# Optimization experiments

Hardware: AMD Instinct MI355X
Metric: run time of the kernel (lower is better)

The kernel has to match this reference:

```python
import jax, jax.numpy as jnp
import numpy as np

N_NODES = 100000
N_EDGES = 1_600_000
D_IN = 128
D_OUT = 128


def setup_inputs() -> dict:
    key = jax.random.key(0)
    k1, k2, k3, k4 = jax.random.split(key, 4)
    x = jax.random.normal(k1, (N_NODES, D_IN), dtype=jnp.float32)
    adj = jax.random.randint(k2, (2, N_EDGES), 0, N_NODES, dtype=jnp.int64)
    # eqx.nn.Linear-style init: U(-1/sqrt(in), 1/sqrt(in))
    lim = 1.0 / np.sqrt(D_IN)
    W = jax.random.uniform(k3, (D_OUT, D_IN), minval=-lim, maxval=lim, dtype=jnp.float32)
    b = jax.random.uniform(k4, (D_OUT,), minval=-lim, maxval=lim, dtype=jnp.float32)
    return {"x": x, "adj": adj, "W": W, "b": b}


def reference(x, adj, W, b):
    n = x.shape[0]
    s, r = adj[0], adj[1]
    ones = jnp.ones(s.shape, dtype=x.dtype)
    sender_degree = jax.ops.segment_sum(ones, s, num_segments=n)    # [n]
    receiver_degree = jax.ops.segment_sum(ones, r, num_segments=n)  # [n]
    # linear (dropout is identity at p=0)
    h = x @ W.T + b                                                 # [n, D_OUT]
    # symmetric degree normalization: rescale senders, scatter-add to receivers, rescale receivers
    h = h * jax.lax.rsqrt(jnp.maximum(sender_degree, 1.0))[:, None]
    h = jax.ops.segment_sum(h[s], r, num_segments=n)                # gather + scatter-add
    h = h * jax.lax.rsqrt(jnp.maximum(receiver_degree, 1.0))[:, None]
    h = jax.nn.silu(h)
    return (h, adj)
```

## Files before the change

### kernel.cpp

```cpp
#include <hip/hip_runtime.h>
#include <hip/hip_bf16.h>
#include <hip/hip_fp16.h>

typedef __attribute__((ext_vector_type(8))) short short8;
typedef __attribute__((ext_vector_type(4))) float floatx4;

#define DFEAT 128
#define BCAP 5120
#define WSTR 136

__device__ __forceinline__ int clampi(int v, int lo, int hi) {
    return v < lo ? lo : (v > hi ? hi : v);
}
__device__ __forceinline__ ushort f2bf(float f) {
    unsigned u = __float_as_uint(f);
    unsigned r = (u + 0x7FFFu + ((u >> 16) & 1u)) >> 16;
    return (ushort)r;
}
__device__ __forceinline__ float bf2f(ushort u) {
    return __uint_as_float(((unsigned)u) << 16);
}
__device__ __forceinline__ float h16tof(ushort hb) {
    __half_raw hr; hr.x = hb;
    return __half2float((__half)hr);
}
__device__ __forceinline__ unsigned f2bf8_sw(float f) {
    __half h = __float2half(f);
    __half_raw hr = (__half_raw)h;
    unsigned u = (unsigned)hr.x;
    return (u + 0x7Fu + ((u >> 8) & 1u)) >> 8;
}
__device__ __forceinline__ unsigned packbf8x4(float4 v) {
#if __has_builtin(__builtin_amdgcn_cvt_pk_bf8_f32)
    int lo = __builtin_amdgcn_cvt_pk_bf8_f32(v.x, v.y, 0, false);
    int full = __builtin_amdgcn_cvt_pk_bf8_f32(v.z, v.w, lo, true);
    return (unsigned)full;
#else
    return f2bf8_sw(v.x) | (f2bf8_sw(v.y) << 8) | (f2bf8_sw(v.z) << 16) | (f2bf8_sw(v.w) << 24);
#endif
}
__device__ __forceinline__ float2 bf8x2tof(int w) {
#if __has_builtin(__builtin_amdgcn_cvt_pk_f32_bf8)
    typedef __attribute__((ext_vector_type(2))) float f2v;
    f2v r = __builtin_amdgcn_cvt_pk_f32_bf8(w, false);
    float2 o; o.x = r[0]; o.y = r[1];
    return o;
#else
    float2 o;
    o.x = h16tof((ushort)((w & 0xFF) << 8));
    o.y = h16tof((ushort)(w & 0xFF00));
    return o;
#endif
}

__device__ __forceinline__ int ldS(const int* adj, int f, int E, int e) {
    return f ? adj[2 * (size_t)e] : adj[e];
}
__device__ __forceinline__ int ldR(const int* adj, int f, int E, int e) {
    return f ? adj[2 * ((size_t)E + e)] : adj[(size_t)E + e];
}

__global__ __launch_bounds__(512) void k_front(const float* __restrict__ x,
                                               unsigned* __restrict__ xs, int n32, int staged,
                                               const float* __restrict__ W, unsigned* __restrict__ Wb,
                                               const int* __restrict__ adj, int* __restrict__ flag_g,
                                               int* __restrict__ scur, int* __restrict__ rcur,
                                               unsigned char* __restrict__ sbuf, unsigned* __restrict__ rbuf,
                                               int E, int N, int NBK, int SG) {
    int t = threadIdx.x;
    int b = blockIdx.x;
    if (b < SG) {
        if (b == 0) {
            for (int i = t; i < 8192; i += 512) {
                float2 v = ((const float2*)W)[i];
                Wb[i] = (unsigned)f2bf(v.x) | ((unsigned)f2bf(v.y) << 16);
            }
        }
        if (staged) {
            int stride = SG * 512;
            for (int i = b * 512 + t; i < n32; i += stride)
                xs[i] = packbf8x4(((const float4*)x)[i]);
        }
        return;
    }
    __shared__ int hs[512], hr[512], bs[512], br[512];
    __shared__ int fsh;
    int pb = b - SG;
    int PB = gridDim.x - SG;
    if (t < 64) {
        int nz = 0;
        for (int i = t; i < 256; i += 64) nz |= adj[2 * i + 1];
        #pragma unroll
        for (int off = 32; off > 0; off >>= 1) nz |= __shfl_down(nz, off);
        if (t == 0) { fsh = (nz == 0) ? 1 : 0; if (pb == 0) flag_g[0] = fsh; }
    }
    hs[t] = 0; hr[t] = 0;
    __syncthreads();
    int f = fsh;
    int chunk = (E + PB - 1) / PB;
    int e0 = pb * chunk;
    int e1 = min(E, e0 + chunk);
    for (int e = e0 + t; e < e1; e += 512) {
        int s = clampi(ldS(adj, f, E, e), 0, N - 1);
        int r = clampi(ldR(adj, f, E, e), 0, N - 1);
        atomicAdd(&hs[s >> 8], 1);
        atomicAdd(&hr[r >> 8], 1);
    }
    __syncthreads();
    for (int i = t; i < NBK; i += 512) {
        bs[i] = hs[i] ? atomicAdd(&scur[i], hs[i]) : 0;
        br[i] = hr[i] ? atomicAdd(&rcur[i], hr[i]) : 0;
    }
    __syncthreads();
    for (int e = e0 + t; e < e1; e += 512) {
        int s = clampi(ldS(adj, f, E, e), 0, N - 1);
        int r = clampi(ldR(adj, f, E, e), 0, N - 1);
        int ps = atomicAdd(&bs[s >> 8], 1);
        if (ps < BCAP) sbuf[(size_t)(s >> 8) * BCAP + ps] = (unsigned char)(s & 255);
        int pr = atomicAdd(&br[r >> 8], 1);
        if (pr < BCAP) rbuf[(size_t)(r >> 8) * BCAP + pr] = ((unsigned)(r & 255) << 17) | (unsigned)s;
    }
}

__global__ __launch_bounds__(256) void k_invs(const unsigned char* __restrict__ sbuf,
                                              const int* __restrict__ scur,
                                              float* __restrict__ inv_s, int N) {
    __shared__ int h[256];
    int b = blockIdx.x, t = threadIdx.x;
    int sc = min(scur[b], BCAP);
    const unsigned char* sb = sbuf + (size_t)b * BCAP;
    h[t] = 0;
    __syncthreads();
    for (int i = t; i < sc; i += 256) atomicAdd(&h[sb[i]], 1);
    __syncthreads();
    int node = (b << 8) + t;
    if (node < N) inv_s[node] = rsqrtf(fmaxf((float)h[t], 1.0f));
}

__global__ __launch_bounds__(256) void k_sort(unsigned* __restrict__ rbuf,
                                              const int* __restrict__ rcur,
                                              const float* __restrict__ inv_s,
                                              int* __restrict__ deg_r, int* __restrict__ startv,
                                              int N) {
    __shared__ unsigned pk[BCAP];
    __shared__ int h[256], off[256];
    int b = blockIdx.x, t = threadIdx.x;
    int node = (b << 8) + t;
    int cnt = min(rcur[b], BCAP);
    unsigned* rb = rbuf + (size_t)b * BCAP;
    for (int i = t; i < cnt; i += 256) pk[i] = rb[i];
    h[t] = 0;
    __syncthreads();
    for (int i = t; i < cnt; i += 256) atomicAdd(&h[pk[i] >> 17], 1);
    __syncthreads();
    int hv = h[t];
    off[t] = hv;
    __syncthreads();
    for (int o = 1; o < 256; o <<= 1) {
        int v = (t >= o) ? off[t - o] : 0;
        __syncthreads();
        off[t] += v;
        __syncthreads();
    }
    int excl = off[t] - hv;
    if (node < N) { deg_r[node] = hv; startv[node] = b * BCAP + excl; }
    __syncthreads();
    h[t] = excl;
    __syncthreads();
    for (int i = t; i < cnt; i += 256) {
        unsigned v = pk[i];
        int s = (int)(v & 0x1FFFFu);
        unsigned iv8 = f2bf8_sw(inv_s[clampi(s, 0, N - 1)]);
        int pos = atomicAdd(&h[v >> 17], 1);
        if (pos >= 0 && pos < cnt) rb[pos] = (v & 0x1FFFFu) | (iv8 << 24);
    }
}

__global__ __launch_bounds__(512) void k_back(const ushort* __restrict__ xs,
                                              const float* __restrict__ bias,
                                              const unsigned* __restrict__ Wb,
                                              const int* __restrict__ startv,
                                              const int* __restrict__ deg_r,
                                              const unsigned* __restrict__ esrc,
                                              float* __restrict__ out0, int N, int RB, int ntiles,
                                              const int* __restrict__ adj, const int* __restrict__ flag,
                                              float* __restrict__ out1, int n1) {
    __shared__ ushort Wt[128 * WSTR];
    __shared__ ushort At[32 * WSTR];
    __shared__ float csrow[32], invrow[32];
    int tid = threadIdx.x;

    if ((int)blockIdx.x >= ntiles) {
        int f = flag[0];
        int nb = gridDim.x - ntiles;
        for (int i = ((int)blockIdx.x - ntiles) * 512 + tid; i < n1; i += nb * 512) {
            int v = f ? adj[2 * (size_t)i] : adj[i];
            out1[i] = bf2f(f2bf((float)v));
        }
        return;
    }

    int m0 = blockIdx.x * 32;
    for (int i = tid; i < 8192; i += 512) {
        unsigned v = Wb[i];
        int row = i >> 6, col = (2 * i) & 127;
        *(unsigned*)(&Wt[row * WSTR + col]) = v;
    }

    int w = tid >> 6, d = tid & 63;
    #pragma unroll 1
    for (int k = 0; k < 4; ++k) {
        int nl = w * 4 + k;
        int node = m0 + nl;
        int cnt = 0, base = 0;
        if (node < N) {
            cnt = clampi(deg_r[node], 0, BCAP);
            base = clampi(startv[node], 0, RB - cnt);
        }
        cnt = __builtin_amdgcn_readfirstlane(cnt);
        base = __builtin_amdgcn_readfirstlane(base);
        const unsigned* ep = esrc + base;
        float a0 = 0.f, a1 = 0.f, cs = 0.f;
        int j = 0;
        for (; j + 7 < cnt; j += 8) {
            unsigned q0 = ep[j],     q1 = ep[j + 1], q2 = ep[j + 2], q3 = ep[j + 3];
            unsigned q4 = ep[j + 4], q5 = ep[j + 5], q6 = ep[j + 6], q7 = ep[j + 7];
            int r0 = (int)xs[((q0 & 0x1FFFFu) << 6) + d];
            int r1 = (int)xs[((q1 & 0x1FFFFu) << 6) + d];
            int r2 = (int)xs[((q2 & 0x1FFFFu) << 6) + d];
            int r3 = (int)xs[((q3 & 0x1FFFFu) << 6) + d];
            int r4 = (int)xs[((q4 & 0x1FFFFu) << 6) + d];
            int r5 = (int)xs[((q5 & 0x1FFFFu) << 6) + d];
            int r6 = (int)xs[((q6 & 0x1FFFFu) << 6) + d];
            int r7 = (int)xs[((q7 & 0x1FFFFu) << 6) + d];
            float v0 = h16tof((ushort)((q0 >> 16) & 0xFF00u));
            float v1 = h16tof((ushort)((q1 >> 16) & 0xFF00u));
            float v2 = h16tof((ushort)((q2 >> 16) & 0xFF00u));
            float v3 = h16tof((ushort)((q3 >> 16) & 0xFF00u));
            float v4 = h16tof((ushort)((q4 >> 16) & 0xFF00u));
            float v5 = h16tof((ushort)((q5 >> 16) & 0xFF00u));
            float v6 = h16tof((ushort)((q6 >> 16) & 0xFF00u));
            float v7 = h16tof((ushort)((q7 >> 16) & 0xFF00u));
            float2 f0 = bf8x2tof(r0), f1 = bf8x2tof(r1), f2 = bf8x2tof(r2), f3 = bf8x2tof(r3);
            float2 f4 = bf8x2tof(r4), f5 = bf8x2tof(r5), f6 = bf8x2tof(r6), f7 = bf8x2tof(r7);
            a0 += v0 * f0.x; a1 += v0 * f0.y;
            a0 += v1 * f1.x; a1 += v1 * f1.y;
            a0 += v2 * f2.x; a1 += v2 * f2.y;
            a0 += v3 * f3.x; a1 += v3 * f3.y;
            a0 += v4 * f4.x; a1 += v4 * f4.y;
            a0 += v5 * f5.x; a1 += v5 * f5.y;
            a0 += v6 * f6.x; a1 += v6 * f6.y;
            a0 += v7 * f7.x; a1 += v7 * f7.y;
            cs += ((v0 + v1) + (v2 + v3)) + ((v4 + v5) + (v6 + v7));
        }
        for (; j < cnt; ++j) {
            unsigned q0 = ep[j];
            float v0 = h16tof((ushort)((q0 >> 16) & 0xFF00u));
            float2 f0 = bf8x2tof((int)xs[((q0 & 0x1FFFFu) << 6) + d]);
            a0 += v0 * f0.x; a1 += v0 * f0.y;
            cs += v0;
        }
        ushort2 p; p.x = f2bf(a0); p.y = f2bf(a1);
        *(ushort2*)(&At[nl * WSTR + 2 * d]) = p;
        if (d == 0) {
            csrow[nl] = cs;
            invrow[nl] = rsqrtf(fmaxf((float)cnt, 1.0f));
        }
    }
    __syncthreads();

    int quad = d >> 4, r16 = d & 15;
    int rt = w & 1;
    short8 a[4];
    #pragma unroll
    for (int g = 0; g < 4; ++g)
        a[g] = *(const short8*)(&At[(rt * 16 + r16) * WSTR + g * 32 + quad * 8]);

    #pragma unroll
    for (int half = 0; half < 2; ++half) {
        int ct = (w >> 1) + half * 4;
        floatx4 acc = {0.f, 0.f, 0.f, 0.f};
        #pragma unroll
        for (int g = 0; g < 4; ++g) {
            short8 bb = *(const short8*)(&Wt[(ct * 16 + r16) * WSTR + g * 32 + quad * 8]);
            acc = __builtin_amdgcn_mfma_f32_16x16x32_bf16(a[g], bb, acc, 0, 0, 0);
        }
        int dcol = ct * 16 + r16;
        float bc = bias[dcol];
        #pragma unroll
        for (int g = 0; g < 4; ++g) {
            int ml = rt * 16 + quad * 4 + g;
            int grow = m0 + ml;
            if (grow < N) {
                float v = (acc[g] + csrow[ml] * bc) * invrow[ml];
                float z = v / (1.0f + __expf(-v));
                if (!(z > -50.0f && z < 50.0f)) z = 0.0f;
                out0[(size_t)grow * DFEAT + dcol] = z;
            }
        }
    }
}

__global__ __launch_bounds__(256) void k_aggregate_fb(const float* __restrict__ x,
                                                      const int* __restrict__ startv,
                                                      const int* __restrict__ deg_r,
                                                      const unsigned* __restrict__ esrc,
                                                      float* __restrict__ xa,
                                                      float* __restrict__ cvec, int N, int RB) {
    int node = blockIdx.x * 4 + (threadIdx.x >> 6);
    int d = threadIdx.x & 63;
    if (node >= N) return;
    int cnt = clampi(deg_r[node], 0, BCAP);
    int base = clampi(startv[node], 0, RB - cnt);
    cnt = __builtin_amdgcn_readfirstlane(cnt);
    base = __builtin_amdgcn_readfirstlane(base);
    const unsigned* ep = esrc + base;
    float a0 = 0.f, a1 = 0.f, cs = 0.f;
    for (int j = 0; j < cnt; ++j) {
        unsigned w0 = ep[j];
        int s0 = (int)(w0 & 0x1FFFFu);
        float v0 = h16tof((ushort)((w0 >> 16) & 0xFF00u));
        float2 f0 = ((const float2*)x)[(size_t)s0 * 64 + d];
        a0 += v0 * f0.x; a1 += v0 * f0.y;
        cs += v0;
    }
    float2 o; o.x = a0; o.y = a1;
    ((float2*)xa)[(size_t)node * 64 + d] = o;
    if (d == 0) cvec[node] = cs;
}

__global__ __launch_bounds__(256) void k_matmul_fb(float* __restrict__ xa,
                                                   const unsigned* __restrict__ Wb,
                                                   const float* __restrict__ bias,
                                                   const float* __restrict__ c,
                                                   const int* __restrict__ deg_r, int M) {
    __shared__ ushort Wt[128 * WSTR];
    __shared__ ushort At[64 * WSTR];
    int tid = threadIdx.x;
    int m0 = blockIdx.x * 64;
    for (int i = tid; i < 8192; i += 256) {
        unsigned v = Wb[i];
        int row = i >> 6, col = (2 * i) & 127;
        *(unsigned*)(&Wt[row * WSTR + col]) = v;
    }
    for (int i = tid; i < 4096; i += 256) {
        int row = i >> 6, col = (2 * i) & 127;
        int grow = m0 + row;
        float2 v;
        if (grow < M) v = ((const float2*)xa)[(size_t)grow * 64 + (col >> 1)];
        else { v.x = 0.f; v.y = 0.f; }
        ushort2 p; p.x = f2bf(v.x); p.y = f2bf(v.y);
        *(ushort2*)(&At[row * WSTR + col]) = p;
    }
    __syncthreads();
    int wid = tid >> 6, lane = tid & 63;
    int quad = lane >> 4, r16 = lane & 15;
    short8 a[4];
    #pragma unroll
    for (int g = 0; g < 4; ++g)
        a[g] = *(const short8*)(&At[(wid * 16 + r16) * WSTR + g * 32 + quad * 8]);
    int rbl = wid * 16 + quad * 4;
    float cg[4], invr[4];
    #pragma unroll
    for (int g = 0; g < 4; ++g) {
        int row = min(m0 + rbl + g, M - 1);
        cg[g] = c[row];
        invr[g] = rsqrtf(fmaxf((float)deg_r[row], 1.0f));
    }
    #pragma unroll
    for (int nt = 0; nt < 8; ++nt) {
        floatx4 acc = {0.f, 0.f, 0.f, 0.f};
        #pragma unroll
        for (int g = 0; g < 4; ++g) {
            short8 bb = *(const short8*)(&Wt[(nt * 16 + r16) * WSTR + g * 32 + quad * 8]);
            acc = __builtin_amdgcn_mfma_f32_16x16x32_bf16(a[g], bb, acc, 0, 0, 0);
        }
        int dcol = nt * 16 + r16;
        float bc = bias[dcol];
        #pragma unroll
        for (int g = 0; g < 4; ++g) {
            int grow = m0 + rbl + g;
            if (grow < M) {
                float v = (acc[g] + cg[g] * bc) * invr[g];
                float z = v / (1.0f + __expf(-v));
                if (!(z > -50.0f && z < 50.0f)) z = 0.0f;
                xa[(size_t)grow * DFEAT + dcol] = z;
            }
        }
    }
}

__global__ void k_adjcopy(const int* __restrict__ adj, const int* __restrict__ flag,
                          float* __restrict__ out, int n) {
    int i = blockIdx.x * 256 + threadIdx.x;
    if (i >= n) return;
    int f = flag[0];
    int v = f ? adj[2 * (size_t)i] : adj[i];
    out[i] = bf2f(f2bf((float)v));
}

extern "C" void kernel_launch(void* const* d_in, const int* in_sizes, int n_in,
                              void* d_out, int out_size, void* d_ws, size_t ws_size,
                              hipStream_t stream) {
    const float* x    = (const float*)d_in[0];
    const int*   adj  = (const int*)d_in[1];
    const float* W    = (const float*)d_in[2];
    const float* bias = (const float*)d_in[3];

    const int N = in_sizes[0] / DFEAT;
    const int E = (out_size - N * DFEAT) / 2;
    const int NBK = (N + 255) >> 8;
    const int N4 = ((N + 255) / 256) * 256;
    const int RB = NBK * BCAP;

    float* out  = (float*)d_out;
    float* out0 = out;
    float* out1 = out + (size_t)N * DFEAT;

    size_t xsB  = (size_t)N * DFEAT;
    size_t sbB  = ((size_t)NBK * BCAP + 255) & ~(size_t)255;
    size_t rbB  = (size_t)RB * 4;
    size_t metaB = (size_t)N4 * 16 + 8192;
    size_t need = xsB + sbB + rbB + metaB + 32768;
    int staged = (ws_size >= need) ? 1 : 0;

    unsigned char* sbuf;
    unsigned* rbuf;
    char* csr;
    ushort* xs = (ushort*)d_ws;
    if (staged) {
        sbuf = (unsigned char*)d_ws + xsB;
        rbuf = (unsigned*)((char*)d_ws + xsB + sbB);
        csr  = (char*)d_ws + xsB + sbB + rbB;
    } else {
        sbuf = (unsigned char*)d_out;
        rbuf = (unsigned*)out1;
        csr  = (char*)out1 + rbB;
    }
    float* inv_s  = (float*)csr;
    int*   deg_r  = (int*)(csr + (size_t)N4 * 4);
    int*   startv = (int*)(csr + (size_t)N4 * 8);
    float* cvec   = (float*)(csr + (size_t)N4 * 12);
    int*   bkt    = (int*)(csr + (size_t)N4 * 16);
    unsigned* Wb  = (unsigned*)(csr + metaB);
    int *scur = bkt, *rcur = bkt + 512, *flag = bkt + 1024;

    hipMemsetAsync(bkt, 0, 1028 * 4, stream);

    int SG = staged ? 512 : 1;
    int PB = 256;
    k_front<<<SG + PB, 512, 0, stream>>>(x, (unsigned*)xs, N * 32, staged, W, Wb, adj, flag,
                                         scur, rcur, sbuf, rbuf, E, N, NBK, SG);
    k_invs<<<NBK, 256, 0, stream>>>(sbuf, scur, inv_s, N);
    k_sort<<<NBK, 256, 0, stream>>>(rbuf, rcur, inv_s, deg_r, startv, N);

    if (staged) {
        int ntiles = (N + 31) / 32;
        k_back<<<ntiles + 256, 512, 0, stream>>>(xs, bias, Wb, startv, deg_r, rbuf,
                                                 out0, N, RB, ntiles, adj, flag, out1, 2 * E);
    } else {
        k_aggregate_fb<<<(N + 3) / 4, 256, 0, stream>>>(x, startv, deg_r, rbuf, out0, cvec, N, RB);
        k_matmul_fb<<<(N + 63) / 64, 256, 0, stream>>>(out0, Wb, bias, cvec, deg_r, N);
        k_adjcopy<<<(2 * E + 255) / 256, 256, 0, stream>>>(adj, flag, out1, 2 * E);
    }
}
```

Measured before the change: 233.4 us.

## Count sender degrees with global atomics, drop k_invs, read W from global

Sender degrees are now counted with direct global atomics in k_front, replacing the bucketed sender buffer and the separate k_invs kernel. The per-receiver coefficient sum moves into k_sort, so the aggregation loop in k_back no longer accumulates it. k_back stops staging W in shared memory, reading MFMA B operands straight from global/L2, and gets a launch bound of 512 threads with a minimum of 8 blocks to raise occupancy. The trade-off is 1.6M contended global atomics and uncached-in-LDS weight reads in exchange for one fewer kernel, less shared memory and higher occupancy.

```diff
diff --git a/kernel.cpp b/kernel.cpp
--- a/kernel.cpp
+++ b/kernel.cpp
@@ -64,8 +64,8 @@
                                                unsigned* __restrict__ xs, int n32, int staged,
                                                const float* __restrict__ W, unsigned* __restrict__ Wb,
                                                const int* __restrict__ adj, int* __restrict__ flag_g,
-                                               int* __restrict__ scur, int* __restrict__ rcur,
-                                               unsigned char* __restrict__ sbuf, unsigned* __restrict__ rbuf,
+                                               int* __restrict__ rcur, int* __restrict__ deg_s,
+                                               unsigned* __restrict__ rbuf,
                                                int E, int N, int NBK, int SG) {
     int t = threadIdx.x;
     int b = blockIdx.x;
@@ -83,7 +83,7 @@
         }
         return;
     }
-    __shared__ int hs[512], hr[512], bs[512], br[512];
+    __shared__ int hr[512], br[512];
     __shared__ int fsh;
     int pb = b - SG;
     int PB = gridDim.x - SG;
@@ -94,62 +94,48 @@
         for (int off = 32; off > 0; off >>= 1) nz |= __shfl_down(nz, off);
         if (t == 0) { fsh = (nz == 0) ? 1 : 0; if (pb == 0) flag_g[0] = fsh; }
     }
-    hs[t] = 0; hr[t] = 0;
+    hr[t] = 0;
     __syncthreads();
     int f = fsh;
     int chunk = (E + PB - 1) / PB;
     int e0 = pb * chunk;
     int e1 = min(E, e0 + chunk);
     for (int e = e0 + t; e < e1; e += 512) {
-        int s = clampi(ldS(adj, f, E, e), 0, N - 1);
         int r = clampi(ldR(adj, f, E, e), 0, N - 1);
-        atomicAdd(&hs[s >> 8], 1);
         atomicAdd(&hr[r >> 8], 1);
     }
     __syncthreads();
-    for (int i = t; i < NBK; i += 512) {
-        bs[i] = hs[i] ? atomicAdd(&scur[i], hs[i]) : 0;
+    for (int i = t; i < NBK; i += 512)
         br[i] = hr[i] ? atomicAdd(&rcur[i], hr[i]) : 0;
-    }
     __syncthreads();
     for (int e = e0 + t; e < e1; e += 512) {
         int s = clampi(ldS(adj, f, E, e), 0, N - 1);
         int r = clampi(ldR(adj, f, E, e), 0, N - 1);
-        int ps = atomicAdd(&bs[s >> 8], 1);
-        if (ps < BCAP) sbuf[(size_t)(s >> 8) * BCAP + ps] = (unsigned char)(s & 255);
+        atomicAdd(&deg_s[s], 1);
         int pr = atomicAdd(&br[r >> 8], 1);
         if (pr < BCAP) rbuf[(size_t)(r >> 8) * BCAP + pr] = ((unsigned)(r & 255) << 17) | (unsigned)s;
     }
 }
 
-__global__ __launch_bounds__(256) void k_invs(const unsigned char* __restrict__ sbuf,
-                                              const int* __restrict__ scur,
-                                              float* __restrict__ inv_s, int N) {
-    __shared__ int h[256];
-    int b = blockIdx.x, t = threadIdx.x;
-    int sc = min(scur[b], BCAP);
-    const unsigned char* sb = sbuf + (size_t)b * BCAP;
-    h[t] = 0;
-    __syncthreads();
-    for (int i = t; i < sc; i += 256) atomicAdd(&h[sb[i]], 1);
-    __syncthreads();
-    int node = (b << 8) + t;
-    if (node < N) inv_s[node] = rsqrtf(fmaxf((float)h[t], 1.0f));
-}
-
 __global__ __launch_bounds__(256) void k_sort(unsigned* __restrict__ rbuf,
                                               const int* __restrict__ rcur,
-                                              const float* __restrict__ inv_s,
+                                              const int* __restrict__ deg_s,
+                                              float* __restrict__ cvec,
                                               int* __restrict__ deg_r, int* __restrict__ startv,
                                               int N) {
-    __shared__ unsigned pk[BCAP];
+    __shared__ __align__(16) unsigned pk[BCAP];
     __shared__ int h[256], off[256];
+    __shared__ float csf[256];
     int b = blockIdx.x, t = threadIdx.x;
     int node = (b << 8) + t;
     int cnt = min(rcur[b], BCAP);
     unsigned* rb = rbuf + (size_t)b * BCAP;
-    for (int i = t; i < cnt; i += 256) pk[i] = rb[i];
+    int cnt4 = cnt >> 2;
+    const uint4* rb4 = (const uint4*)rb;
+    for (int i = t; i < cnt4; i += 256) ((uint4*)pk)[i] = rb4[i];
+    for (int i = (cnt4 << 2) + t; i < cnt; i += 256) pk[i] = rb[i];
     h[t] = 0;
+    csf[t] = 0.f;
     __syncthreads();
     for (int i = t; i < cnt; i += 256) atomicAdd(&h[pk[i] >> 17], 1);
     __syncthreads();
@@ -170,22 +156,27 @@
     for (int i = t; i < cnt; i += 256) {
         unsigned v = pk[i];
         int s = (int)(v & 0x1FFFFu);
-        unsigned iv8 = f2bf8_sw(inv_s[clampi(s, 0, N - 1)]);
+        int dg = deg_s[clampi(s, 0, N - 1)];
+        unsigned iv8 = f2bf8_sw(rsqrtf(fmaxf((float)dg, 1.0f)));
+        float vq = h16tof((ushort)(iv8 << 8));
+        atomicAdd(&csf[v >> 17], vq);
         int pos = atomicAdd(&h[v >> 17], 1);
         if (pos >= 0 && pos < cnt) rb[pos] = (v & 0x1FFFFu) | (iv8 << 24);
     }
-}
-
-__global__ __launch_bounds__(512) void k_back(const ushort* __restrict__ xs,
-                                              const float* __restrict__ bias,
-                                              const unsigned* __restrict__ Wb,
-                                              const int* __restrict__ startv,
-                                              const int* __restrict__ deg_r,
-                                              const unsigned* __restrict__ esrc,
-                                              float* __restrict__ out0, int N, int RB, int ntiles,
-                                              const int* __restrict__ adj, const int* __restrict__ flag,
-                                              float* __restrict__ out1, int n1) {
-    __shared__ ushort Wt[128 * WSTR];
+    __syncthreads();
+    if (node < N) cvec[node] = csf[t];
+}
+
+__global__ __launch_bounds__(512, 8) void k_back(const ushort* __restrict__ xs,
+                                                 const float* __restrict__ bias,
+                                                 const unsigned* __restrict__ Wb,
+                                                 const int* __restrict__ startv,
+                                                 const int* __restrict__ deg_r,
+                                                 const unsigned* __restrict__ esrc,
+                                                 const float* __restrict__ cvec,
+                                                 float* __restrict__ out0, int N, int RB, int ntiles,
+                                                 const int* __restrict__ adj, const int* __restrict__ flag,
+                                                 float* __restrict__ out1, int n1) {
     __shared__ ushort At[32 * WSTR];
     __shared__ float csrow[32], invrow[32];
     int tid = threadIdx.x;
@@ -201,12 +192,6 @@
     }
 
     int m0 = blockIdx.x * 32;
-    for (int i = tid; i < 8192; i += 512) {
-        unsigned v = Wb[i];
-        int row = i >> 6, col = (2 * i) & 127;
-        *(unsigned*)(&Wt[row * WSTR + col]) = v;
-    }
-
     int w = tid >> 6, d = tid & 63;
     #pragma unroll 1
     for (int k = 0; k < 4; ++k) {
@@ -220,7 +205,7 @@
         cnt = __builtin_amdgcn_readfirstlane(cnt);
         base = __builtin_amdgcn_readfirstlane(base);
         const unsigned* ep = esrc + base;
-        float a0 = 0.f, a1 = 0.f, cs = 0.f;
+        float a0 = 0.f, a1 = 0.f;
         int j = 0;
         for (; j + 7 < cnt; j += 8) {
             unsigned q0 = ep[j],     q1 = ep[j + 1], q2 = ep[j + 2], q3 = ep[j + 3];
@@ -251,19 +236,17 @@
             a0 += v5 * f5.x; a1 += v5 * f5.y;
             a0 += v6 * f6.x; a1 += v6 * f6.y;
             a0 += v7 * f7.x; a1 += v7 * f7.y;
-            cs += ((v0 + v1) + (v2 + v3)) + ((v4 + v5) + (v6 + v7));
         }
         for (; j < cnt; ++j) {
             unsigned q0 = ep[j];
             float v0 = h16tof((ushort)((q0 >> 16) & 0xFF00u));
             float2 f0 = bf8x2tof((int)xs[((q0 & 0x1FFFFu) << 6) + d]);
             a0 += v0 * f0.x; a1 += v0 * f0.y;
-            cs += v0;
         }
         ushort2 p; p.x = f2bf(a0); p.y = f2bf(a1);
         *(ushort2*)(&At[nl * WSTR + 2 * d]) = p;
         if (d == 0) {
-            csrow[nl] = cs;
+            csrow[nl] = (node < N) ? cvec[node] : 0.f;
             invrow[nl] = rsqrtf(fmaxf((float)cnt, 1.0f));
         }
     }
@@ -276,13 +259,14 @@
     for (int g = 0; g < 4; ++g)
         a[g] = *(const short8*)(&At[(rt * 16 + r16) * WSTR + g * 32 + quad * 8]);
 
+    const ushort* Wr = (const ushort*)Wb;
     #pragma unroll
     for (int half = 0; half < 2; ++half) {
         int ct = (w >> 1) + half * 4;
         floatx4 acc = {0.f, 0.f, 0.f, 0.f};
         #pragma unroll
         for (int g = 0; g < 4; ++g) {
-            short8 bb = *(const short8*)(&Wt[(ct * 16 + r16) * WSTR + g * 32 + quad * 8]);
+            short8 bb = *(const short8*)(Wr + ((ct * 16 + r16) << 7) + g * 32 + quad * 8);
             acc = __builtin_amdgcn_mfma_f32_16x16x32_bf16(a[g], bb, acc, 0, 0, 0);
         }
         int dcol = ct * 16 + r16;
@@ -305,8 +289,7 @@
                                                       const int* __restrict__ startv,
                                                       const int* __restrict__ deg_r,
                                                       const unsigned* __restrict__ esrc,
-                                                      float* __restrict__ xa,
-                                                      float* __restrict__ cvec, int N, int RB) {
+                                                      float* __restrict__ xa, int N, int RB) {
     int node = blockIdx.x * 4 + (threadIdx.x >> 6);
     int d = threadIdx.x & 63;
     if (node >= N) return;
@@ -315,18 +298,16 @@
     cnt = __builtin_amdgcn_readfirstlane(cnt);
     base = __builtin_amdgcn_readfirstlane(base);
     const unsigned* ep = esrc + base;
-    float a0 = 0.f, a1 = 0.f, cs = 0.f;
+    float a0 = 0.f, a1 = 0.f;
     for (int j = 0; j < cnt; ++j) {
         unsigned w0 = ep[j];
         int s0 = (int)(w0 & 0x1FFFFu);
         float v0 = h16tof((ushort)((w0 >> 16) & 0xFF00u));
         float2 f0 = ((const float2*)x)[(size_t)s0 * 64 + d];
         a0 += v0 * f0.x; a1 += v0 * f0.y;
-        cs += v0;
     }
     float2 o; o.x = a0; o.y = a1;
     ((float2*)xa)[(size_t)node * 64 + d] = o;
-    if (d == 0) cvec[node] = cs;
 }
 
 __global__ __launch_bounds__(256) void k_matmul_fb(float* __restrict__ xa,
@@ -418,48 +399,44 @@
     float* out1 = out + (size_t)N * DFEAT;
 
     size_t xsB  = (size_t)N * DFEAT;
-    size_t sbB  = ((size_t)NBK * BCAP + 255) & ~(size_t)255;
     size_t rbB  = (size_t)RB * 4;
-    size_t metaB = (size_t)N4 * 16 + 8192;
-    size_t need = xsB + sbB + rbB + metaB + 32768;
+    size_t metaB = (size_t)N4 * 16 + 4096 + 32768;
+    size_t need = xsB + rbB + metaB + 4096;
     int staged = (ws_size >= need) ? 1 : 0;
 
-    unsigned char* sbuf;
     unsigned* rbuf;
     char* csr;
     ushort* xs = (ushort*)d_ws;
     if (staged) {
-        sbuf = (unsigned char*)d_ws + xsB;
-        rbuf = (unsigned*)((char*)d_ws + xsB + sbB);
-        csr  = (char*)d_ws + xsB + sbB + rbB;
+        rbuf = (unsigned*)((char*)d_ws + xsB);
+        csr  = (char*)d_ws + xsB + rbB;
     } else {
-        sbuf = (unsigned char*)d_out;
         rbuf = (unsigned*)out1;
         csr  = (char*)out1 + rbB;
     }
-    float* inv_s  = (float*)csr;
-    int*   deg_r  = (int*)(csr + (size_t)N4 * 4);
-    int*   startv = (int*)(csr + (size_t)N4 * 8);
-    float* cvec   = (float*)(csr + (size_t)N4 * 12);
-    int*   bkt    = (int*)(csr + (size_t)N4 * 16);
-    unsigned* Wb  = (unsigned*)(csr + metaB);
-    int *scur = bkt, *rcur = bkt + 512, *flag = bkt + 1024;
-
-    hipMemsetAsync(bkt, 0, 1028 * 4, stream);
+    int*   ibase  = (int*)csr;
+    int*   deg_s  = ibase;
+    int*   rcur   = ibase + N4;
+    int*   flag   = ibase + N4 + 512;
+    int*   deg_r  = ibase + N4 + 1024;
+    int*   startv = deg_r + N4;
+    float* cvec   = (float*)(startv + N4);
+    unsigned* Wb  = (unsigned*)(cvec + N4);
+
+    hipMemsetAsync(deg_s, 0, (size_t)N4 * 4 + 4096, stream);
 
     int SG = staged ? 512 : 1;
     int PB = 256;
     k_front<<<SG + PB, 512, 0, stream>>>(x, (unsigned*)xs, N * 32, staged, W, Wb, adj, flag,
-                                         scur, rcur, sbuf, rbuf, E, N, NBK, SG);
-    k_invs<<<NBK, 256, 0, stream>>>(sbuf, scur, inv_s, N);
-    k_sort<<<NBK, 256, 0, stream>>>(rbuf, rcur, inv_s, deg_r, startv, N);
+                                         rcur, deg_s, rbuf, E, N, NBK, SG);
+    k_sort<<<NBK, 256, 0, stream>>>(rbuf, rcur, deg_s, cvec, deg_r, startv, N);
 
     if (staged) {
         int ntiles = (N + 31) / 32;
-        k_back<<<ntiles + 256, 512, 0, stream>>>(xs, bias, Wb, startv, deg_r, rbuf,
+        k_back<<<ntiles + 256, 512, 0, stream>>>(xs, bias, Wb, startv, deg_r, rbuf, cvec,
                                                  out0, N, RB, ntiles, adj, flag, out1, 2 * E);
     } else {
-        k_aggregate_fb<<<(N + 3) / 4, 256, 0, stream>>>(x, startv, deg_r, rbuf, out0, cvec, N, RB);
+        k_aggregate_fb<<<(N + 3) / 4, 256, 0, stream>>>(x, startv, deg_r, rbuf, out0, N, RB);
         k_matmul_fb<<<(N + 63) / 64, 256, 0, stream>>>(out0, Wb, bias, cvec, deg_r, N);
         k_adjcopy<<<(2 * E + 255) / 256, 256, 0, stream>>>(adj, flag, out1, 2 * E);
     }
```

Result: slower. 276.9 us (+18.7%).
